# Kernel tuning notes

Measured on AMD Instinct MI355X. Metric: run time of the kernel, lower is better.

The kernel has to match this reference:

```python
import jax, jax.numpy as jnp
import numpy as np

R, TOTAL, N_NODE, B = 4, 32768, 1024, 32
D_IN, D_HID, C, H, NCLS = 256, 256, 8, 8, 10
E = 262144


def setup_inputs() -> dict:
    key = jax.random.key(0)
    ks = jax.random.split(key, 20)
    s = 0.05  # weight scale for numerical stability
    return {
        "h": jax.random.normal(ks[0], (TOTAL, D_IN), jnp.float32),
        "src": jax.random.randint(ks[1], (R, E), 0, TOTAL),
        "dst": jax.random.randint(ks[2], (R, E), 0, TOTAL),
        "node_label": jax.random.randint(ks[3], (TOTAL,), 0, C),
        "feat_label": jax.random.randint(ks[4], (D_HID,), 0, C),
        "W1": jax.random.normal(ks[5], (R, D_IN, D_HID), jnp.float32) * s,
        "b1": jnp.zeros((R, D_HID), jnp.float32),
        "W2": jax.random.normal(ks[6], (R, D_HID, D_HID), jnp.float32) * s,
        "b2": jnp.zeros((R, D_HID), jnp.float32),
        "Wr": jax.random.normal(ks[7], (C, D_HID, D_HID), jnp.float32) * s,
        "br": jnp.zeros((C, D_HID), jnp.float32),
        "Wq": jax.random.normal(ks[8], (D_HID, D_HID), jnp.float32) * s,
        "Wk": jax.random.normal(ks[9], (D_HID, D_HID), jnp.float32) * s,
        "Wv": jax.random.normal(ks[10], (D_HID, D_HID), jnp.float32) * s,
        "lin_w": jax.random.normal(ks[11], (D_HID, D_HID), jnp.float32) * s,
        "lin_b": jnp.zeros((D_HID,), jnp.float32),
        "bn_gamma": jnp.ones((D_HID,), jnp.float32),
        "bn_beta": jnp.zeros((D_HID,), jnp.float32),
        "cls_w": jax.random.normal(ks[12], (NCLS, D_HID), jnp.float32) * s,
        "cls_b": jnp.zeros((NCLS,), jnp.float32),
    }


def _gconv(x, src, dst, W, b, n):
    # DGL GraphConv norm='both' with self-loops added (dgl.add_self_loop)
    loop = jnp.arange(n)
    s = jnp.concatenate([src, loop])
    d = jnp.concatenate([dst, loop])
    ones = jnp.ones(s.shape, jnp.float32)
    deg_out = jnp.maximum(jax.ops.segment_sum(ones, s, num_segments=n), 1.0)
    deg_in = jnp.maximum(jax.ops.segment_sum(ones, d, num_segments=n), 1.0)
    msg = x[s] * jax.lax.rsqrt(deg_out)[s][:, None]          # [E+n, D]
    agg = jax.ops.segment_sum(msg, d, num_segments=n)        # [n, D]
    agg = agg * jax.lax.rsqrt(deg_in)[:, None]
    return agg @ W + b


def _hetero_layer(x, src, dst, W, b, n):
    # HeteroGraphConv: per-relation GraphConv, 'sum' cross-relation aggregation
    out = 0.0
    for r in range(R):
        out = out + _gconv(x, src[r], dst[r], W[r], b[r], n)
    return out


def _attention(x, Wq, Wk, Wv, lin_w, lin_b):
    # FeatureAttentionLayer (eval mode: no attn dropout)
    b, c, d = x.shape
    dh = d // H
    q = (x @ Wq).reshape(b, c, H, dh).transpose(2, 0, 1, 3)   # [H,B,C,dh]
    k = (x @ Wk).reshape(b, c, H, dh).transpose(2, 0, 1, 3)
    v = (x @ Wv).reshape(b, c, H, dh).transpose(2, 0, 1, 3)
    scores = jnp.einsum('hbqd,hbkd->hbqk', q, k) / jnp.sqrt(jnp.float32(c))
    attn = jax.nn.softmax(scores, axis=-1)
    o = jnp.einsum('hbqk,hbkd->hbqd', attn, v)
    o = o.transpose(1, 2, 0, 3).reshape(b, c, d)              # [B,C,D]
    ff = jax.nn.relu(o @ lin_w.T + lin_b) + o                 # feedforward + inner residual
    out = ff + x                                              # outer residual
    return jnp.mean(out, axis=1)                              # [B,D]


def reference(h, src, dst, node_label, feat_label, W1, b1, W2, b2, Wr, br,
              Wq, Wk, Wv, lin_w, lin_b, bn_gamma, bn_beta, cls_w, cls_b):
    n = h.shape[0]
    # RGCN: conv1 -> relu -> conv2
    h1 = jax.nn.relu(_hetero_layer(h, src, dst, W1, b1, n))
    h2 = _hetero_layer(h1, src, dst, W2, b2, n)               # [TOTAL, D_HID]

    node_emb = h2.reshape(B, N_NODE, D_HID)
    node_mask0 = node_label.reshape(B, N_NODE)[0]             # first graph's node types

    # cluster-wise masked pooling + per-cluster linear resize
    pooled = []
    for key in range(C):
        fmask = (feat_label == key).astype(h2.dtype)          # [D]
        nmask = (node_mask0 == key).astype(h2.dtype)          # [N]
        cnt = jnp.maximum(nmask.sum(), 1.0)
        v = jnp.einsum('bnd,n->bd', node_emb, nmask) / cnt    # mean over cluster's nodes
        v = v * fmask[None, :]                                # keep only cluster's features
        pooled.append(v @ Wr[key].T + br[key])
    emb_in = jnp.stack(pooled, axis=1)                        # [B, C, D]

    graph_emb = _attention(emb_in, Wq, Wk, Wv, lin_w, lin_b)  # [B, D]

    hg_raw = jnp.mean(node_emb, axis=1)                       # dgl.mean_nodes per graph
    diff = graph_emb.reshape(-1) - hg_raw.reshape(-1)
    recon = jnp.sqrt(jnp.sum(jnp.square(diff + 1e-6)))        # pairwise_distance p=2

    # BatchNorm1d with batch statistics, dropout identity (eval)
    mu = jnp.mean(graph_emb, axis=0)
    var = jnp.var(graph_emb, axis=0)
    hg = (graph_emb - mu) * jax.lax.rsqrt(var + 1e-5) * bn_gamma + bn_beta
    logits = hg @ cls_w.T + cls_b                             # [B, NCLS]
    return logits, recon
```

## Files before the change

kernel.cpp:

```cpp
#include <hip/hip_runtime.h>
#include <math.h>

#define R_ 4
#define TOTAL_ 32768
#define NNODE_ 1024
#define B_ 32
#define DH_ 256
#define C_ 8
#define H_ 8
#define NCLS_ 10
#define E_ 262144
#define S_ 32
#define CHUNK_ (E_ / S_)

typedef __attribute__((ext_vector_type(8))) short short8v;
typedef __attribute__((ext_vector_type(8))) unsigned short u16x8;
typedef __attribute__((ext_vector_type(4))) float f32x4;
typedef __attribute__((ext_vector_type(2))) float f32x2;
typedef __attribute__((ext_vector_type(2))) unsigned int uint2v;

__device__ inline unsigned short f2bf(float f) {
  unsigned int u = __builtin_bit_cast(unsigned int, f);
  u += 0x7FFF + ((u >> 16) & 1);
  return (unsigned short)(u >> 16);
}
__device__ inline float bf2f(unsigned short s) {
  return __builtin_bit_cast(float, (unsigned int)s << 16);
}


__global__ __launch_bounds__(1024) void hist_part(const int* __restrict__ src,
                                                  const int* __restrict__ dst,
                                                  unsigned int* __restrict__ parts) {
  int r = blockIdx.y, s = blockIdx.x, t = threadIdx.x;
  __shared__ unsigned int hs[16384], hd[16384];
  for (int i = t; i < 16384; i += 1024) { hs[i] = 0; hd[i] = 0; }
  __syncthreads();
  const int* sp = src + (size_t)r * E_ + s * CHUNK_;
  const int* dp = dst + (size_t)r * E_ + s * CHUNK_;
  for (int i = t; i < CHUNK_; i += 1024) {
    int a = sp[i], b = dp[i];
    atomicAdd(&hs[a >> 1], 1u << ((a & 1) * 16));
    atomicAdd(&hd[b >> 1], 1u << ((b & 1) * 16));
  }
  __syncthreads();
  unsigned int* po = parts + ((size_t)(r * S_ + s) * 2) * 16384;
  for (int i = t; i < 16384; i += 1024) { po[i] = hs[i]; po[16384 + i] = hd[i]; }
}

__global__ void reduce_deg(const unsigned int* __restrict__ parts,
                           float* __restrict__ rs_out, float* __restrict__ rs_in,
                           int* __restrict__ cnt_in) {
  int gid = blockIdx.x * 256 + threadIdx.x;
  int r = gid >> 14, w = gid & 16383;
  unsigned int s0 = 0, s1 = 0, d0 = 0, d1 = 0;
  for (int s = 0; s < S_; s++) {
    unsigned int ws_ = parts[((size_t)(r * S_ + s) * 2) * 16384 + w];
    unsigned int wd  = parts[((size_t)(r * S_ + s) * 2 + 1) * 16384 + w];
    s0 += ws_ & 0xffff; s1 += ws_ >> 16;
    d0 += wd & 0xffff;  d1 += wd >> 16;
  }
  int n0 = w * 2, n1 = n0 + 1;
  rs_out[r * TOTAL_ + n0] = rsqrtf((float)(s0 + 1));
  rs_out[r * TOTAL_ + n1] = rsqrtf((float)(s1 + 1));
  rs_in[r * TOTAL_ + n0]  = rsqrtf((float)(d0 + 1));
  rs_in[r * TOTAL_ + n1]  = rsqrtf((float)(d1 + 1));
  cnt_in[r * TOTAL_ + n0] = (int)d0;
  cnt_in[r * TOTAL_ + n1] = (int)d1;
}

__global__ __launch_bounds__(1024) void scan_counts(const int* __restrict__ cnt_in,
                                                    int* __restrict__ off) {
  int r = blockIdx.x;
  const int* c = cnt_in + r * TOTAL_;
  int* o = off + r * (TOTAL_ + 1);
  __shared__ int part[1024];
  int t = threadIdx.x;
  int base = t * 32;
  int loc[32];
  int s = 0;
#pragma unroll
  for (int j = 0; j < 32; j++) { loc[j] = c[base + j]; s += loc[j]; }
  part[t] = s;
  __syncthreads();
  for (int d = 1; d < 1024; d <<= 1) {
    int v = (t >= d) ? part[t - d] : 0;
    __syncthreads();
    part[t] += v;
    __syncthreads();
  }
  int run = (t == 0) ? 0 : part[t - 1];
#pragma unroll
  for (int j = 0; j < 32; j++) {
    o[base + j] = run;
    run += loc[j];
  }
  if (t == 1023) o[TOTAL_] = run;
}

__global__ void base_gen(const unsigned int* __restrict__ parts,
                         const int* __restrict__ csr_off,
                         unsigned int* __restrict__ sbb) {
  int gid = blockIdx.x * 256 + threadIdx.x;
  int r = gid >> 14, w = gid & 16383;
  int n0 = w * 2, n1 = n0 + 1;
  unsigned int run0 = (unsigned int)csr_off[r * (TOTAL_ + 1) + n0];
  unsigned int run1 = (unsigned int)csr_off[r * (TOTAL_ + 1) + n1];
  for (int s = 0; s < S_; s++) {
    unsigned int wd = parts[((size_t)(r * S_ + s) * 2 + 1) * 16384 + w];
    sbb[(size_t)(r * S_ + s) * TOTAL_ + n0] = run0;
    sbb[(size_t)(r * S_ + s) * TOTAL_ + n1] = run1;
    run0 += wd & 0xffff;
    run1 += wd >> 16;
  }
}

__global__ __launch_bounds__(1024) void scatter_csr(const int* __restrict__ src,
                                                    const int* __restrict__ dst,
                                                    const unsigned int* __restrict__ sbb,
                                                    int* __restrict__ csr_src) {
  int r = blockIdx.y, s = blockIdx.x, t = threadIdx.x;
  __shared__ unsigned int basel[TOTAL_];
  const unsigned int* sb = sbb + (size_t)(r * S_ + s) * TOTAL_;
  for (int i = t; i < TOTAL_; i += 1024) basel[i] = sb[i];
  __syncthreads();
  const int* sp = src + (size_t)r * E_ + s * CHUNK_;
  const int* dp = dst + (size_t)r * E_ + s * CHUNK_;
  int* co = csr_src + (size_t)r * E_;
  for (int i = t; i < CHUNK_; i += 1024) {
    int d = dp[i];
    unsigned int slot = atomicAdd(&basel[d], 1u);
    co[slot] = sp[i];
  }
}


__global__ void hconv8(const float* __restrict__ x, unsigned int* __restrict__ xq) {
  size_t i = (size_t)blockIdx.x * blockDim.x + threadIdx.x;
  float4 a = ((const float4*)x)[2 * i];
  float4 b = ((const float4*)x)[2 * i + 1];
  unsigned int lo = 0, hi = 0;
  lo = __builtin_amdgcn_cvt_pk_fp8_f32(a.x, a.y, lo, false);
  lo = __builtin_amdgcn_cvt_pk_fp8_f32(a.z, a.w, lo, true);
  hi = __builtin_amdgcn_cvt_pk_fp8_f32(b.x, b.y, hi, false);
  hi = __builtin_amdgcn_cvt_pk_fp8_f32(b.z, b.w, hi, true);
  uint2v o; o[0] = lo; o[1] = hi;
  *(uint2v*)&xq[2 * i] = o;
}

__global__ void wconv2(const float* __restrict__ W1, const float* __restrict__ W2,
                       unsigned short* __restrict__ T1, unsigned short* __restrict__ T2) {
  int i = blockIdx.x * blockDim.x + threadIdx.x;
  const float* W = (i < 262144) ? W1 : W2;
  unsigned short* T = (i < 262144) ? T1 : T2;
  int j = i & 262143;
  int k = j >> 8, c = j & 255;
  T[(size_t)c * 1024 + k] = f2bf(W[j]);
}

__global__ void bias_sum2(const float* __restrict__ b1, const float* __restrict__ b2,
                          float* __restrict__ s1, float* __restrict__ s2) {
  const float* b = blockIdx.x ? b2 : b1;
  float* s = blockIdx.x ? s2 : s1;
  int d = threadIdx.x;
  s[d] = b[d] + b[DH_ + d] + b[2 * DH_ + d] + b[3 * DH_ + d];
}

__global__ void transpose_mats(const float* __restrict__ Wr, const float* __restrict__ lw,
                               float* __restrict__ Wrt, float* __restrict__ lwt) {
  int i = blockIdx.x * blockDim.x + threadIdx.x;
  int m = i >> 16, j = i & 65535;
  int row = j >> 8, col = j & 255;
  float v = (m < 8) ? Wr[(size_t)m * 65536 + j] : lw[j];
  float* T = (m < 8) ? (Wrt + (size_t)m * 65536) : lwt;
  T[col * 256 + row] = v;
}

__global__ __launch_bounds__(256) void aggregate_f8(
    const unsigned int* __restrict__ xq, const int* __restrict__ csr_off,
    const int* __restrict__ csr_src, const float* __restrict__ rs_out,
    const float* __restrict__ rs_in, unsigned short* __restrict__ aggB) {
  int r = blockIdx.y;
  int node = blockIdx.x * 8 + (threadIdx.x >> 5);
  int lane5 = threadIdx.x & 31;
  const int* offr = csr_off + r * (TOTAL_ + 1);
  const int* srcs = csr_src + (size_t)r * E_;
  const float* rso = rs_out + r * TOTAL_;
  float acc[8];
  {
    uint2v v = *(const uint2v*)&xq[(size_t)node * 64 + lane5 * 2];
    float w = rso[node];
    f32x2 p;
    p = __builtin_amdgcn_cvt_pk_f32_fp8(v[0], false); acc[0] = p[0] * w; acc[1] = p[1] * w;
    p = __builtin_amdgcn_cvt_pk_f32_fp8(v[0], true);  acc[2] = p[0] * w; acc[3] = p[1] * w;
    p = __builtin_amdgcn_cvt_pk_f32_fp8(v[1], false); acc[4] = p[0] * w; acc[5] = p[1] * w;
    p = __builtin_amdgcn_cvt_pk_f32_fp8(v[1], true);  acc[6] = p[0] * w; acc[7] = p[1] * w;
  }
  int e0 = offr[node], e1 = offr[node + 1];
  int e = e0;
  for (; e + 2 <= e1; e += 2) {
    int s0 = srcs[e], s1 = srcs[e + 1];
    uint2v v0 = *(const uint2v*)&xq[(size_t)s0 * 64 + lane5 * 2];
    uint2v v1 = *(const uint2v*)&xq[(size_t)s1 * 64 + lane5 * 2];
    float w0 = rso[s0], w1 = rso[s1];
    f32x2 p;
    p = __builtin_amdgcn_cvt_pk_f32_fp8(v0[0], false); acc[0] += p[0] * w0; acc[1] += p[1] * w0;
    p = __builtin_amdgcn_cvt_pk_f32_fp8(v0[0], true);  acc[2] += p[0] * w0; acc[3] += p[1] * w0;
    p = __builtin_amdgcn_cvt_pk_f32_fp8(v0[1], false); acc[4] += p[0] * w0; acc[5] += p[1] * w0;
    p = __builtin_amdgcn_cvt_pk_f32_fp8(v0[1], true);  acc[6] += p[0] * w0; acc[7] += p[1] * w0;
    p = __builtin_amdgcn_cvt_pk_f32_fp8(v1[0], false); acc[0] += p[0] * w1; acc[1] += p[1] * w1;
    p = __builtin_amdgcn_cvt_pk_f32_fp8(v1[0], true);  acc[2] += p[0] * w1; acc[3] += p[1] * w1;
    p = __builtin_amdgcn_cvt_pk_f32_fp8(v1[1], false); acc[4] += p[0] * w1; acc[5] += p[1] * w1;
    p = __builtin_amdgcn_cvt_pk_f32_fp8(v1[1], true);  acc[6] += p[0] * w1; acc[7] += p[1] * w1;
  }
  if (e < e1) {
    int s0 = srcs[e];
    uint2v v0 = *(const uint2v*)&xq[(size_t)s0 * 64 + lane5 * 2];
    float w0 = rso[s0];
    f32x2 p;
    p = __builtin_amdgcn_cvt_pk_f32_fp8(v0[0], false); acc[0] += p[0] * w0; acc[1] += p[1] * w0;
    p = __builtin_amdgcn_cvt_pk_f32_fp8(v0[0], true);  acc[2] += p[0] * w0; acc[3] += p[1] * w0;
    p = __builtin_amdgcn_cvt_pk_f32_fp8(v0[1], false); acc[4] += p[0] * w0; acc[5] += p[1] * w0;
    p = __builtin_amdgcn_cvt_pk_f32_fp8(v0[1], true);  acc[6] += p[0] * w0; acc[7] += p[1] * w0;
  }
  float wi = rs_in[r * TOTAL_ + node];
  u16x8 o;
#pragma unroll
  for (int j = 0; j < 8; j++) o[j] = f2bf(acc[j] * wi);
  *(u16x8*)&aggB[(size_t)node * 1024 + r * DH_ + lane5 * 8] = o;
}

template <int MODE>
__global__ __launch_bounds__(256) void gemm_mfma(
    const unsigned short* __restrict__ A, const unsigned short* __restrict__ Bt,
    const float* __restrict__ bias, unsigned char* __restrict__ out8,
    unsigned short* __restrict__ out16) {
  __shared__ unsigned short As[128][40];
  __shared__ unsigned short Bs[128][40];
  int t = threadIdx.x;
  int row0 = blockIdx.x * 128, col0 = blockIdx.y * 128;
  int wid = t >> 6, lane = t & 63;
  int wm = wid >> 1, wn = wid & 1;
  int lr = lane & 15, lk = (lane >> 4) * 8;
  f32x4 acc[4][4] = {};
  for (int k0 = 0; k0 < 1024; k0 += 32) {
#pragma unroll
    for (int i = 0; i < 2; i++) {
      int chunk = t + 256 * i;
      int rr = chunk >> 2, kc = (chunk & 3) * 8;
      short8v av = *(const short8v*)&A[(size_t)(row0 + rr) * 1024 + k0 + kc];
      *(short8v*)&As[rr][kc] = av;
      short8v bv = *(const short8v*)&Bt[(size_t)(col0 + rr) * 1024 + k0 + kc];
      *(short8v*)&Bs[rr][kc] = bv;
    }
    __syncthreads();
    short8v afr[4], bfr[4];
#pragma unroll
    for (int m = 0; m < 4; m++) afr[m] = *(const short8v*)&As[wm * 64 + m * 16 + lr][lk];
#pragma unroll
    for (int n = 0; n < 4; n++) bfr[n] = *(const short8v*)&Bs[wn * 64 + n * 16 + lr][lk];
#pragma unroll
    for (int m = 0; m < 4; m++)
#pragma unroll
      for (int n = 0; n < 4; n++)
        acc[m][n] = __builtin_amdgcn_mfma_f32_16x16x32_bf16(afr[m], bfr[n], acc[m][n], 0, 0, 0);
    __syncthreads();
  }
  int lq = lane >> 4;
#pragma unroll
  for (int m = 0; m < 4; m++) {
    int row = row0 + wm * 64 + m * 16 + lq * 4;
#pragma unroll
    for (int n = 0; n < 4; n++) {
      int col = col0 + wn * 64 + n * 16 + lr;
      float bv = bias[col];
#pragma unroll
      for (int q = 0; q < 4; q++) {
        float v = acc[m][n][q] + bv;
        if (MODE == 0) {
          v = fmaxf(v, 0.f);
          int b8 = __builtin_amdgcn_cvt_pk_fp8_f32(v, 0.f, 0, false);
          out8[(size_t)(row + q) * DH_ + col] = (unsigned char)b8;
        } else {
          out16[(size_t)(row + q) * DH_ + col] = f2bf(v);
        }
      }
    }
  }
}


__global__ __launch_bounds__(256) void pool_part(const unsigned short* __restrict__ h2b,
                                                 const int* __restrict__ node_label,
                                                 float* __restrict__ part) {
  int b = blockIdx.x, ch = blockIdx.y, d = threadIdx.x;
  __shared__ int slab[128];
  if (d < 128) slab[d] = node_label[ch * 128 + d];
  __syncthreads();
  float a[C_] = {0.f};
  float at = 0.f;
  const unsigned short* base = h2b + ((size_t)b * NNODE_ + ch * 128) * DH_ + d;
  for (int n = 0; n < 128; n++) {
    float x = bf2f(base[(size_t)n * DH_]);
    int lab = slab[n];
    at += x;
#pragma unroll
    for (int k = 0; k < C_; k++) a[k] += (lab == k) ? x : 0.f;
  }
  float* pb = part + ((size_t)(ch * B_ + b) * 9) * DH_ + d;
#pragma unroll
  for (int k = 0; k < C_; k++) pb[(size_t)k * DH_] = a[k];
  pb[(size_t)8 * DH_] = at;
}

__global__ __launch_bounds__(256) void pool_fin(const float* __restrict__ part,
                                                const int* __restrict__ node_label,
                                                const int* __restrict__ feat_label,
                                                float* __restrict__ poolv,
                                                float* __restrict__ hg_raw) {
  int b = blockIdx.x, d = threadIdx.x;
  __shared__ int cnt[C_];
  if (d < C_) cnt[d] = 0;
  __syncthreads();
  for (int n = d; n < NNODE_; n += 256) atomicAdd(&cnt[node_label[n]], 1);
  __syncthreads();
  float s[9];
#pragma unroll
  for (int k = 0; k < 9; k++) s[k] = 0.f;
  for (int ch = 0; ch < 8; ch++) {
    const float* pb = part + ((size_t)(ch * B_ + b) * 9) * DH_ + d;
#pragma unroll
    for (int k = 0; k < 9; k++) s[k] += pb[(size_t)k * DH_];
  }
  int fl = feat_label[d];
#pragma unroll
  for (int k = 0; k < C_; k++) {
    float cntf = fmaxf((float)cnt[k], 1.f);
    float v = (fl == k) ? (s[k] / cntf) : 0.f;
    poolv[((size_t)k * B_ + b) * DH_ + d] = v;
  }
  hg_raw[(size_t)b * DH_ + d] = s[8] * (1.f / NNODE_);
}


__global__ __launch_bounds__(256) void resize_t(const float* __restrict__ poolv,
                                                const float* __restrict__ Wrt,
                                                const float* __restrict__ br,
                                                float* __restrict__ emb) {
  int key = blockIdx.x & 7, b = blockIdx.x >> 3, t = threadIdx.x;
  __shared__ float pl[DH_];
  pl[t] = poolv[((size_t)key * B_ + b) * DH_ + t];
  __syncthreads();
  const float* W = Wrt + (size_t)key * DH_ * DH_;
  float s = 0.f;
  for (int d = 0; d < DH_; d++) s += pl[d] * W[d * DH_ + t];
  emb[((size_t)b * C_ + key) * DH_ + t] = s + br[key * DH_ + t];
}

__global__ __launch_bounds__(256) void qkv_t(const float* __restrict__ emb,
                                             const float* __restrict__ Wq,
                                             const float* __restrict__ Wk,
                                             const float* __restrict__ Wv,
                                             float* __restrict__ q, float* __restrict__ k,
                                             float* __restrict__ v) {
  int idx = blockIdx.x, t = threadIdx.x;
  __shared__ float x[DH_];
  x[t] = emb[(size_t)idx * DH_ + t];
  __syncthreads();
  float sq = 0.f, sk = 0.f, sv = 0.f;
  for (int kk = 0; kk < DH_; kk++) {
    float xv = x[kk];
    sq += xv * Wq[kk * DH_ + t];
    sk += xv * Wk[kk * DH_ + t];
    sv += xv * Wv[kk * DH_ + t];
  }
  q[(size_t)idx * DH_ + t] = sq;
  k[(size_t)idx * DH_ + t] = sk;
  v[(size_t)idx * DH_ + t] = sv;
}

__global__ __launch_bounds__(256) void attn_core(const float* __restrict__ q,
                                                 const float* __restrict__ k,
                                                 const float* __restrict__ v,
                                                 float* __restrict__ osb) {
  int b = blockIdx.x, t = threadIdx.x;
  __shared__ float qs[C_][DH_], ks[C_][DH_], vs[C_][DH_];
  __shared__ float sc[H_][C_][C_];
  for (int c = 0; c < C_; c++) {
    qs[c][t] = q[((size_t)b * C_ + c) * DH_ + t];
    ks[c][t] = k[((size_t)b * C_ + c) * DH_ + t];
    vs[c][t] = v[((size_t)b * C_ + c) * DH_ + t];
  }
  __syncthreads();
  for (int idx = t; idx < H_ * C_ * C_; idx += 256) {
    int hh = idx / (C_ * C_);
    int qc = (idx / C_) % C_;
    int kc = idx % C_;
    float s = 0.f;
    for (int dd = 0; dd < 32; dd++) s += qs[qc][hh * 32 + dd] * ks[kc][hh * 32 + dd];
    sc[hh][qc][kc] = s * 0.35355339059327373f;
  }
  __syncthreads();
  if (t < H_ * C_) {
    int hh = t / C_, qc = t % C_;
    float m = -1e30f;
    for (int kc = 0; kc < C_; kc++) m = fmaxf(m, sc[hh][qc][kc]);
    float sum = 0.f;
    for (int kc = 0; kc < C_; kc++) { float e = expf(sc[hh][qc][kc] - m); sc[hh][qc][kc] = e; sum += e; }
    float inv = 1.f / sum;
    for (int kc = 0; kc < C_; kc++) sc[hh][qc][kc] *= inv;
  }
  __syncthreads();
  int hh = t >> 5;
  for (int c = 0; c < C_; c++) {
    float s = 0.f;
#pragma unroll
    for (int kc = 0; kc < C_; kc++) s += sc[hh][c][kc] * vs[kc][t];
    osb[((size_t)b * C_ + c) * DH_ + t] = s;
  }
}

__global__ __launch_bounds__(256) void ff_res(const float* __restrict__ osb,
                                              const float* __restrict__ emb,
                                              const float* __restrict__ lwt,
                                              const float* __restrict__ lb,
                                              float* __restrict__ ffb) {
  int idx = blockIdx.x, t = threadIdx.x;
  __shared__ float ox[DH_];
  ox[t] = osb[(size_t)idx * DH_ + t];
  __syncthreads();
  float s = 0.f;
  for (int d = 0; d < DH_; d++) s += ox[d] * lwt[d * DH_ + t];
  ffb[(size_t)idx * DH_ + t] =
      fmaxf(s + lb[t], 0.f) + ox[t] + emb[(size_t)idx * DH_ + t];
}

__global__ __launch_bounds__(256) void tail_final(
    const float* __restrict__ ffb, const float* __restrict__ hg_raw,
    const float* __restrict__ g, const float* __restrict__ be,
    const float* __restrict__ cw, const float* __restrict__ cb,
    float* __restrict__ out) {
  int t = threadIdx.x;
  __shared__ float hgn[B_][DH_];
  __shared__ float red[256];
  float gcol[B_];
  float mu = 0.f;
#pragma unroll
  for (int b = 0; b < B_; b++) {
    float s = 0.f;
    for (int c = 0; c < C_; c++) s += ffb[((size_t)b * C_ + c) * DH_ + t];
    gcol[b] = s * (1.f / C_);
    mu += gcol[b];
  }
  mu *= (1.f / B_);
  float var = 0.f;
#pragma unroll
  for (int b = 0; b < B_; b++) { float x = gcol[b] - mu; var += x * x; }
  var *= (1.f / B_);
  float is = rsqrtf(var + 1e-5f);
  float gm = g[t], bt = be[t];
  float s = 0.f;
#pragma unroll
  for (int b = 0; b < B_; b++) {
    hgn[b][t] = (gcol[b] - mu) * is * gm + bt;
    float d = gcol[b] - hg_raw[b * DH_ + t] + 1e-6f;
    s += d * d;
  }
  red[t] = s;
  __syncthreads();
  for (int w = 128; w > 0; w >>= 1) {
    if (t < w) red[t] += red[t + w];
    __syncthreads();
  }
  if (t == 0) out[B_ * NCLS_] = sqrtf(red[0]);
  for (int o = t; o < B_ * NCLS_; o += 256) {
    int b = o / NCLS_, j = o % NCLS_;
    float sl = cb[j];
    for (int d = 0; d < DH_; d++) sl += hgn[b][d] * cw[j * DH_ + d];
    out[o] = sl;
  }
}


extern "C" void kernel_launch(void* const* d_in, const int* in_sizes, int n_in,
                              void* d_out, int out_size, void* d_ws, size_t ws_size,
                              hipStream_t stream) {
  const float* h   = (const float*)d_in[0];
  const int* src   = (const int*)d_in[1];
  const int* dst   = (const int*)d_in[2];
  const int* nlab  = (const int*)d_in[3];
  const int* flab  = (const int*)d_in[4];
  const float* W1  = (const float*)d_in[5];
  const float* b1  = (const float*)d_in[6];
  const float* W2  = (const float*)d_in[7];
  const float* b2  = (const float*)d_in[8];
  const float* Wr  = (const float*)d_in[9];
  const float* br  = (const float*)d_in[10];
  const float* Wq  = (const float*)d_in[11];
  const float* Wk  = (const float*)d_in[12];
  const float* Wv  = (const float*)d_in[13];
  const float* lw  = (const float*)d_in[14];
  const float* lb  = (const float*)d_in[15];
  const float* bng = (const float*)d_in[16];
  const float* bnb = (const float*)d_in[17];
  const float* cw  = (const float*)d_in[18];
  const float* cb  = (const float*)d_in[19];
  float* out = (float*)d_out;

  char* p = (char*)d_ws;
  auto alloc = [&](size_t bytes) -> void* {
    void* q = (void*)p;
    p += (bytes + 255) & ~(size_t)255;
    return q;
  };
  unsigned int* xq    = (unsigned int*)alloc((size_t)TOTAL_ * DH_);
  unsigned char* h1q  = (unsigned char*)alloc((size_t)TOTAL_ * DH_);
  unsigned short* h2b = (unsigned short*)alloc((size_t)TOTAL_ * DH_ * 2);
  unsigned short* aggB = (unsigned short*)alloc((size_t)TOTAL_ * 1024 * 2);
  unsigned short* Wt1  = (unsigned short*)alloc((size_t)1024 * DH_ * 2);
  unsigned short* Wt2  = (unsigned short*)alloc((size_t)1024 * DH_ * 2);
  float* Wrt   = (float*)alloc((size_t)C_ * DH_ * DH_ * 4);
  float* lwt   = (float*)alloc((size_t)DH_ * DH_ * 4);
  float* bsum1 = (float*)alloc(DH_ * 4);
  float* bsum2 = (float*)alloc(DH_ * 4);
  int* cnt_in   = (int*)alloc((size_t)R_ * TOTAL_ * 4);
  float* rs_out = (float*)alloc((size_t)R_ * TOTAL_ * 4);
  float* rs_in  = (float*)alloc((size_t)R_ * TOTAL_ * 4);
  int* csr_off  = (int*)alloc((size_t)R_ * (TOTAL_ + 1) * 4);
  int* csr_src  = (int*)alloc((size_t)R_ * E_ * 4);
  float* part   = (float*)alloc((size_t)8 * B_ * 9 * DH_ * 4);
  float* poolv  = (float*)alloc((size_t)C_ * B_ * DH_ * 4);
  float* hg_raw = (float*)alloc((size_t)B_ * DH_ * 4);
  float* emb    = (float*)alloc((size_t)B_ * C_ * DH_ * 4);
  float* qb     = (float*)alloc((size_t)B_ * C_ * DH_ * 4);
  float* kb     = (float*)alloc((size_t)B_ * C_ * DH_ * 4);
  float* vb     = (float*)alloc((size_t)B_ * C_ * DH_ * 4);
  float* osb    = (float*)alloc((size_t)B_ * C_ * DH_ * 4);
  float* ffb    = (float*)alloc((size_t)B_ * C_ * DH_ * 4);

  unsigned int* parts = (unsigned int*)aggB;
  unsigned int* sbb   = (unsigned int*)((char*)aggB + (size_t)16 * 1024 * 1024);

  hist_part<<<dim3(S_, R_), 1024, 0, stream>>>(src, dst, parts);
  reduce_deg<<<R_ * TOTAL_ / 512, 256, 0, stream>>>(parts, rs_out, rs_in, cnt_in);
  scan_counts<<<R_, 1024, 0, stream>>>(cnt_in, csr_off);
  base_gen<<<R_ * TOTAL_ / 512, 256, 0, stream>>>(parts, csr_off, sbb);
  scatter_csr<<<dim3(S_, R_), 1024, 0, stream>>>(src, dst, sbb, csr_src);

  wconv2<<<2048, 256, 0, stream>>>(W1, W2, Wt1, Wt2);
  bias_sum2<<<2, 256, 0, stream>>>(b1, b2, bsum1, bsum2);
  transpose_mats<<<9 * 256, 256, 0, stream>>>(Wr, lw, Wrt, lwt);
  hconv8<<<TOTAL_ * DH_ / 8 / 256, 256, 0, stream>>>(h, xq);

  aggregate_f8<<<dim3(TOTAL_ / 8, R_), 256, 0, stream>>>(xq, csr_off, csr_src, rs_out, rs_in, aggB);
  gemm_mfma<0><<<dim3(TOTAL_ / 128, 2), 256, 0, stream>>>(aggB, Wt1, bsum1, h1q, nullptr);

  aggregate_f8<<<dim3(TOTAL_ / 8, R_), 256, 0, stream>>>((const unsigned int*)h1q, csr_off, csr_src, rs_out, rs_in, aggB);
  gemm_mfma<1><<<dim3(TOTAL_ / 128, 2), 256, 0, stream>>>(aggB, Wt2, bsum2, nullptr, h2b);

  pool_part<<<dim3(B_, 8), 256, 0, stream>>>(h2b, nlab, part);
  pool_fin<<<B_, 256, 0, stream>>>(part, nlab, flab, poolv, hg_raw);
  resize_t<<<B_ * C_, 256, 0, stream>>>(poolv, Wrt, br, emb);
  qkv_t<<<B_ * C_, 256, 0, stream>>>(emb, Wq, Wk, Wv, qb, kb, vb);
  attn_core<<<B_, 256, 0, stream>>>(qb, kb, vb, osb);
  ff_res<<<B_ * C_, 256, 0, stream>>>(osb, emb, lwt, lb, ffb);
  tail_final<<<1, 256, 0, stream>>>(ffb, hg_raw, bng, bnb, cw, cb, out);
}
```

Measured before the change: 320.7 us.

## Switch aggregation output and layer GEMMs from bf16 to fp8 MFMA

The aggregation kernel now writes its normalized sums as fp8 instead of bf16, using one 64-lane wave per node. Both layer GEMMs consume these fp8 inputs with fp8-quantized weights through the fp8 MFMA instruction, processing 64-wide K steps. This halves the aggregation write traffic and the GEMM read traffic and uses the higher-throughput fp8 matrix path, at the cost of extra quantization error on aggregated features and weights. The resize and QKV projection kernels are also fused into one launch, which removes an emb round trip.

Measured after the change: 330.1 us. 1.03x slower.

```diff
diff --git a/kernel.cpp b/kernel.cpp
--- a/kernel.cpp
+++ b/kernel.cpp
@@ -13,11 +13,11 @@
 #define S_ 32
 #define CHUNK_ (E_ / S_)
 
-typedef __attribute__((ext_vector_type(8))) short short8v;
-typedef __attribute__((ext_vector_type(8))) unsigned short u16x8;
 typedef __attribute__((ext_vector_type(4))) float f32x4;
 typedef __attribute__((ext_vector_type(2))) float f32x2;
 typedef __attribute__((ext_vector_type(2))) unsigned int uint2v;
+typedef __attribute__((ext_vector_type(4))) unsigned int uint4v;
+typedef long long i64;
 
 __device__ inline unsigned short f2bf(float f) {
   unsigned int u = __builtin_bit_cast(unsigned int, f);
@@ -148,14 +148,22 @@
   *(uint2v*)&xq[2 * i] = o;
 }
 
-__global__ void wconv2(const float* __restrict__ W1, const float* __restrict__ W2,
-                       unsigned short* __restrict__ T1, unsigned short* __restrict__ T2) {
-  int i = blockIdx.x * blockDim.x + threadIdx.x;
-  const float* W = (i < 262144) ? W1 : W2;
-  unsigned short* T = (i < 262144) ? T1 : T2;
-  int j = i & 262143;
-  int k = j >> 8, c = j & 255;
-  T[(size_t)c * 1024 + k] = f2bf(W[j]);
+__global__ void wconv_f8(const float* __restrict__ W1, const float* __restrict__ W2,
+                         unsigned int* __restrict__ T1, unsigned int* __restrict__ T2) {
+  int id = blockIdx.x * blockDim.x + threadIdx.x;
+  const float* W = (id < 65536) ? W1 : W2;
+  unsigned int* T = (id < 65536) ? T1 : T2;
+  int j = id & 65535;
+  int c = j >> 8, kq = j & 255;
+  int k0 = kq * 4;
+  float w0 = W[(size_t)(k0 + 0) * 256 + c];
+  float w1 = W[(size_t)(k0 + 1) * 256 + c];
+  float w2 = W[(size_t)(k0 + 2) * 256 + c];
+  float w3 = W[(size_t)(k0 + 3) * 256 + c];
+  unsigned int o = 0;
+  o = __builtin_amdgcn_cvt_pk_fp8_f32(w0, w1, o, false);
+  o = __builtin_amdgcn_cvt_pk_fp8_f32(w2, w3, o, true);
+  T[(size_t)c * 256 + kq] = o;
 }
 
 __global__ void bias_sum2(const float* __restrict__ b1, const float* __restrict__ b2,
@@ -179,91 +187,90 @@
 __global__ __launch_bounds__(256) void aggregate_f8(
     const unsigned int* __restrict__ xq, const int* __restrict__ csr_off,
     const int* __restrict__ csr_src, const float* __restrict__ rs_out,
-    const float* __restrict__ rs_in, unsigned short* __restrict__ aggB) {
+    const float* __restrict__ rs_in, unsigned int* __restrict__ aggQ) {
   int r = blockIdx.y;
-  int node = blockIdx.x * 8 + (threadIdx.x >> 5);
-  int lane5 = threadIdx.x & 31;
+  int node = blockIdx.x * 4 + (threadIdx.x >> 6);
+  int lane = threadIdx.x & 63;
   const int* offr = csr_off + r * (TOTAL_ + 1);
   const int* srcs = csr_src + (size_t)r * E_;
   const float* rso = rs_out + r * TOTAL_;
-  float acc[8];
+  float a0, a1, a2, a3;
   {
-    uint2v v = *(const uint2v*)&xq[(size_t)node * 64 + lane5 * 2];
+    unsigned int v = xq[(size_t)node * 64 + lane];
     float w = rso[node];
-    f32x2 p;
-    p = __builtin_amdgcn_cvt_pk_f32_fp8(v[0], false); acc[0] = p[0] * w; acc[1] = p[1] * w;
-    p = __builtin_amdgcn_cvt_pk_f32_fp8(v[0], true);  acc[2] = p[0] * w; acc[3] = p[1] * w;
-    p = __builtin_amdgcn_cvt_pk_f32_fp8(v[1], false); acc[4] = p[0] * w; acc[5] = p[1] * w;
-    p = __builtin_amdgcn_cvt_pk_f32_fp8(v[1], true);  acc[6] = p[0] * w; acc[7] = p[1] * w;
+    f32x2 p0 = __builtin_amdgcn_cvt_pk_f32_fp8(v, false);
+    f32x2 p1 = __builtin_amdgcn_cvt_pk_f32_fp8(v, true);
+    a0 = p0[0] * w; a1 = p0[1] * w; a2 = p1[0] * w; a3 = p1[1] * w;
   }
   int e0 = offr[node], e1 = offr[node + 1];
   int e = e0;
-  for (; e + 2 <= e1; e += 2) {
-    int s0 = srcs[e], s1 = srcs[e + 1];
-    uint2v v0 = *(const uint2v*)&xq[(size_t)s0 * 64 + lane5 * 2];
-    uint2v v1 = *(const uint2v*)&xq[(size_t)s1 * 64 + lane5 * 2];
-    float w0 = rso[s0], w1 = rso[s1];
+  for (; e + 4 <= e1; e += 4) {
+    int s0 = srcs[e], s1 = srcs[e + 1], s2 = srcs[e + 2], s3 = srcs[e + 3];
+    unsigned int v0 = xq[(size_t)s0 * 64 + lane];
+    unsigned int v1 = xq[(size_t)s1 * 64 + lane];
+    unsigned int v2 = xq[(size_t)s2 * 64 + lane];
+    unsigned int v3 = xq[(size_t)s3 * 64 + lane];
+    float w0 = rso[s0], w1 = rso[s1], w2 = rso[s2], w3 = rso[s3];
     f32x2 p;
-    p = __builtin_amdgcn_cvt_pk_f32_fp8(v0[0], false); acc[0] += p[0] * w0; acc[1] += p[1] * w0;
-    p = __builtin_amdgcn_cvt_pk_f32_fp8(v0[0], true);  acc[2] += p[0] * w0; acc[3] += p[1] * w0;
-    p = __builtin_amdgcn_cvt_pk_f32_fp8(v0[1], false); acc[4] += p[0] * w0; acc[5] += p[1] * w0;
-    p = __builtin_amdgcn_cvt_pk_f32_fp8(v0[1], true);  acc[6] += p[0] * w0; acc[7] += p[1] * w0;
-    p = __builtin_amdgcn_cvt_pk_f32_fp8(v1[0], false); acc[0] += p[0] * w1; acc[1] += p[1] * w1;
-    p = __builtin_amdgcn_cvt_pk_f32_fp8(v1[0], true);  acc[2] += p[0] * w1; acc[3] += p[1] * w1;
-    p = __builtin_amdgcn_cvt_pk_f32_fp8(v1[1], false); acc[4] += p[0] * w1; acc[5] += p[1] * w1;
-    p = __builtin_amdgcn_cvt_pk_f32_fp8(v1[1], true);  acc[6] += p[0] * w1; acc[7] += p[1] * w1;
-  }
-  if (e < e1) {
+    p = __builtin_amdgcn_cvt_pk_f32_fp8(v0, false); a0 += p[0] * w0; a1 += p[1] * w0;
+    p = __builtin_amdgcn_cvt_pk_f32_fp8(v0, true);  a2 += p[0] * w0; a3 += p[1] * w0;
+    p = __builtin_amdgcn_cvt_pk_f32_fp8(v1, false); a0 += p[0] * w1; a1 += p[1] * w1;
+    p = __builtin_amdgcn_cvt_pk_f32_fp8(v1, true);  a2 += p[0] * w1; a3 += p[1] * w1;
+    p = __builtin_amdgcn_cvt_pk_f32_fp8(v2, false); a0 += p[0] * w2; a1 += p[1] * w2;
+    p = __builtin_amdgcn_cvt_pk_f32_fp8(v2, true);  a2 += p[0] * w2; a3 += p[1] * w2;
+    p = __builtin_amdgcn_cvt_pk_f32_fp8(v3, false); a0 += p[0] * w3; a1 += p[1] * w3;
+    p = __builtin_amdgcn_cvt_pk_f32_fp8(v3, true);  a2 += p[0] * w3; a3 += p[1] * w3;
+  }
+  for (; e < e1; e++) {
     int s0 = srcs[e];
-    uint2v v0 = *(const uint2v*)&xq[(size_t)s0 * 64 + lane5 * 2];
+    unsigned int v0 = xq[(size_t)s0 * 64 + lane];
     float w0 = rso[s0];
     f32x2 p;
-    p = __builtin_amdgcn_cvt_pk_f32_fp8(v0[0], false); acc[0] += p[0] * w0; acc[1] += p[1] * w0;
-    p = __builtin_amdgcn_cvt_pk_f32_fp8(v0[0], true);  acc[2] += p[0] * w0; acc[3] += p[1] * w0;
-    p = __builtin_amdgcn_cvt_pk_f32_fp8(v0[1], false); acc[4] += p[0] * w0; acc[5] += p[1] * w0;
-    p = __builtin_amdgcn_cvt_pk_f32_fp8(v0[1], true);  acc[6] += p[0] * w0; acc[7] += p[1] * w0;
+    p = __builtin_amdgcn_cvt_pk_f32_fp8(v0, false); a0 += p[0] * w0; a1 += p[1] * w0;
+    p = __builtin_amdgcn_cvt_pk_f32_fp8(v0, true);  a2 += p[0] * w0; a3 += p[1] * w0;
   }
   float wi = rs_in[r * TOTAL_ + node];
-  u16x8 o;
-#pragma unroll
-  for (int j = 0; j < 8; j++) o[j] = f2bf(acc[j] * wi);
-  *(u16x8*)&aggB[(size_t)node * 1024 + r * DH_ + lane5 * 8] = o;
+  unsigned int o = 0;
+  o = __builtin_amdgcn_cvt_pk_fp8_f32(a0 * wi, a1 * wi, o, false);
+  o = __builtin_amdgcn_cvt_pk_fp8_f32(a2 * wi, a3 * wi, o, true);
+  aggQ[(size_t)node * 256 + r * 64 + lane] = o;
 }
 
 template <int MODE>
-__global__ __launch_bounds__(256) void gemm_mfma(
-    const unsigned short* __restrict__ A, const unsigned short* __restrict__ Bt,
+__global__ __launch_bounds__(256) void gemm_f8(
+    const unsigned char* __restrict__ A, const unsigned char* __restrict__ Bt,
     const float* __restrict__ bias, unsigned char* __restrict__ out8,
     unsigned short* __restrict__ out16) {
-  __shared__ unsigned short As[128][40];
-  __shared__ unsigned short Bs[128][40];
+  __shared__ unsigned char As[128][80];
+  __shared__ unsigned char Bs[128][80];
   int t = threadIdx.x;
   int row0 = blockIdx.x * 128, col0 = blockIdx.y * 128;
   int wid = t >> 6, lane = t & 63;
   int wm = wid >> 1, wn = wid & 1;
-  int lr = lane & 15, lk = (lane >> 4) * 8;
+  int lr = lane & 15, lk = lane >> 4;
   f32x4 acc[4][4] = {};
-  for (int k0 = 0; k0 < 1024; k0 += 32) {
+  for (int k0 = 0; k0 < 1024; k0 += 64) {
 #pragma unroll
     for (int i = 0; i < 2; i++) {
-      int chunk = t + 256 * i;
-      int rr = chunk >> 2, kc = (chunk & 3) * 8;
-      short8v av = *(const short8v*)&A[(size_t)(row0 + rr) * 1024 + k0 + kc];
-      *(short8v*)&As[rr][kc] = av;
-      short8v bv = *(const short8v*)&Bt[(size_t)(col0 + rr) * 1024 + k0 + kc];
-      *(short8v*)&Bs[rr][kc] = bv;
+      int c = t + 256 * i;
+      int rr = c >> 2, cc = (c & 3) * 16;
+      *(uint4v*)&As[rr][cc] = *(const uint4v*)&A[(size_t)(row0 + rr) * 1024 + k0 + cc];
+      *(uint4v*)&Bs[rr][cc] = *(const uint4v*)&Bt[(size_t)(col0 + rr) * 1024 + k0 + cc];
     }
     __syncthreads();
-    short8v afr[4], bfr[4];
-#pragma unroll
-    for (int m = 0; m < 4; m++) afr[m] = *(const short8v*)&As[wm * 64 + m * 16 + lr][lk];
-#pragma unroll
-    for (int n = 0; n < 4; n++) bfr[n] = *(const short8v*)&Bs[wn * 64 + n * 16 + lr][lk];
-#pragma unroll
-    for (int m = 0; m < 4; m++)
-#pragma unroll
-      for (int n = 0; n < 4; n++)
-        acc[m][n] = __builtin_amdgcn_mfma_f32_16x16x32_bf16(afr[m], bfr[n], acc[m][n], 0, 0, 0);
+#pragma unroll
+    for (int kk = 0; kk < 2; kk++) {
+      i64 afr[4], bfr[4];
+#pragma unroll
+      for (int m = 0; m < 4; m++) afr[m] = *(const i64*)&As[wm * 64 + m * 16 + lr][kk * 32 + lk * 8];
+#pragma unroll
+      for (int n = 0; n < 4; n++) bfr[n] = *(const i64*)&Bs[wn * 64 + n * 16 + lr][kk * 32 + lk * 8];
+#pragma unroll
+      for (int m = 0; m < 4; m++)
+#pragma unroll
+        for (int n = 0; n < 4; n++)
+          acc[m][n] = __builtin_amdgcn_mfma_f32_16x16x32_fp8_fp8(afr[m], bfr[n], acc[m][n], 0, 0, 0);
+    }
     __syncthreads();
   }
   int lq = lane >> 4;
@@ -343,40 +350,37 @@
 }
 
 
-__global__ __launch_bounds__(256) void resize_t(const float* __restrict__ poolv,
-                                                const float* __restrict__ Wrt,
-                                                const float* __restrict__ br,
-                                                float* __restrict__ emb) {
+__global__ __launch_bounds__(256) void rq_t(const float* __restrict__ poolv,
+                                            const float* __restrict__ Wrt,
+                                            const float* __restrict__ br,
+                                            const float* __restrict__ Wq,
+                                            const float* __restrict__ Wk,
+                                            const float* __restrict__ Wv,
+                                            float* __restrict__ emb,
+                                            float* __restrict__ q, float* __restrict__ k,
+                                            float* __restrict__ v) {
   int key = blockIdx.x & 7, b = blockIdx.x >> 3, t = threadIdx.x;
-  __shared__ float pl[DH_];
+  __shared__ float pl[DH_], es[DH_];
   pl[t] = poolv[((size_t)key * B_ + b) * DH_ + t];
   __syncthreads();
   const float* W = Wrt + (size_t)key * DH_ * DH_;
   float s = 0.f;
   for (int d = 0; d < DH_; d++) s += pl[d] * W[d * DH_ + t];
-  emb[((size_t)b * C_ + key) * DH_ + t] = s + br[key * DH_ + t];
-}
-
-__global__ __launch_bounds__(256) void qkv_t(const float* __restrict__ emb,
-                                             const float* __restrict__ Wq,
-                                             const float* __restrict__ Wk,
-                                             const float* __restrict__ Wv,
-                                             float* __restrict__ q, float* __restrict__ k,
-                                             float* __restrict__ v) {
-  int idx = blockIdx.x, t = threadIdx.x;
-  __shared__ float x[DH_];
-  x[t] = emb[(size_t)idx * DH_ + t];
+  s += br[key * DH_ + t];
+  es[t] = s;
+  size_t idx = (size_t)b * C_ + key;
+  emb[idx * DH_ + t] = s;
   __syncthreads();
   float sq = 0.f, sk = 0.f, sv = 0.f;
   for (int kk = 0; kk < DH_; kk++) {
-    float xv = x[kk];
+    float xv = es[kk];
     sq += xv * Wq[kk * DH_ + t];
     sk += xv * Wk[kk * DH_ + t];
     sv += xv * Wv[kk * DH_ + t];
   }
-  q[(size_t)idx * DH_ + t] = sq;
-  k[(size_t)idx * DH_ + t] = sk;
-  v[(size_t)idx * DH_ + t] = sv;
+  q[idx * DH_ + t] = sq;
+  k[idx * DH_ + t] = sk;
+  v[idx * DH_ + t] = sv;
 }
 
 __global__ __launch_bounds__(256) void attn_core(const float* __restrict__ q,
@@ -514,11 +518,11 @@
     return q;
   };
   unsigned int* xq    = (unsigned int*)alloc((size_t)TOTAL_ * DH_);
-  unsigned char* h1q  = (unsigned char*)alloc((size_t)TOTAL_ * DH_);
+  unsigned int* h1q   = (unsigned int*)alloc((size_t)TOTAL_ * DH_);
   unsigned short* h2b = (unsigned short*)alloc((size_t)TOTAL_ * DH_ * 2);
-  unsigned short* aggB = (unsigned short*)alloc((size_t)TOTAL_ * 1024 * 2);
-  unsigned short* Wt1  = (unsigned short*)alloc((size_t)1024 * DH_ * 2);
-  unsigned short* Wt2  = (unsigned short*)alloc((size_t)1024 * DH_ * 2);
+  unsigned int* aggQ  = (unsigned int*)alloc((size_t)TOTAL_ * 1024);
+  unsigned int* Wq1   = (unsigned int*)alloc((size_t)256 * 256 * 4);
+  unsigned int* Wq2   = (unsigned int*)alloc((size_t)256 * 256 * 4);
   float* Wrt   = (float*)alloc((size_t)C_ * DH_ * DH_ * 4);
   float* lwt   = (float*)alloc((size_t)DH_ * DH_ * 4);
   float* bsum1 = (float*)alloc(DH_ * 4);
@@ -538,8 +542,8 @@
   float* osb    = (float*)alloc((size_t)B_ * C_ * DH_ * 4);
   float* ffb    = (float*)alloc((size_t)B_ * C_ * DH_ * 4);
 
-  unsigned int* parts = (unsigned int*)aggB;
-  unsigned int* sbb   = (unsigned int*)((char*)aggB + (size_t)16 * 1024 * 1024);
+  unsigned int* parts = aggQ;
+  unsigned int* sbb   = (unsigned int*)((char*)aggQ + (size_t)16 * 1024 * 1024);
 
   hist_part<<<dim3(S_, R_), 1024, 0, stream>>>(src, dst, parts);
   reduce_deg<<<R_ * TOTAL_ / 512, 256, 0, stream>>>(parts, rs_out, rs_in, cnt_in);
@@ -547,21 +551,24 @@
   base_gen<<<R_ * TOTAL_ / 512, 256, 0, stream>>>(parts, csr_off, sbb);
   scatter_csr<<<dim3(S_, R_), 1024, 0, stream>>>(src, dst, sbb, csr_src);
 
-  wconv2<<<2048, 256, 0, stream>>>(W1, W2, Wt1, Wt2);
+  wconv_f8<<<512, 256, 0, stream>>>(W1, W2, Wq1, Wq2);
   bias_sum2<<<2, 256, 0, stream>>>(b1, b2, bsum1, bsum2);
   transpose_mats<<<9 * 256, 256, 0, stream>>>(Wr, lw, Wrt, lwt);
   hconv8<<<TOTAL_ * DH_ / 8 / 256, 256, 0, stream>>>(h, xq);
 
-  aggregate_f8<<<dim3(TOTAL_ / 8, R_), 256, 0, stream>>>(xq, csr_off, csr_src, rs_out, rs_in, aggB);
-  gemm_mfma<0><<<dim3(TOTAL_ / 128, 2), 256, 0, stream>>>(aggB, Wt1, bsum1, h1q, nullptr);
-
-  aggregate_f8<<<dim3(TOTAL_ / 8, R_), 256, 0, stream>>>((const unsigned int*)h1q, csr_off, csr_src, rs_out, rs_in, aggB);
-  gemm_mfma<1><<<dim3(TOTAL_ / 128, 2), 256, 0, stream>>>(aggB, Wt2, bsum2, nullptr, h2b);
+  aggregate_f8<<<dim3(TOTAL_ / 4, R_), 256, 0, stream>>>(xq, csr_off, csr_src, rs_out, rs_in, aggQ);
+  gemm_f8<0><<<dim3(TOTAL_ / 128, 2), 256, 0, stream>>>(
+      (const unsigned char*)aggQ, (const unsigned char*)Wq1, bsum1,
+      (unsigned char*)h1q, nullptr);
+
+  aggregate_f8<<<dim3(TOTAL_ / 4, R_), 256, 0, stream>>>(h1q, csr_off, csr_src, rs_out, rs_in, aggQ);
+  gemm_f8<1><<<dim3(TOTAL_ / 128, 2), 256, 0, stream>>>(
+      (const unsigned char*)aggQ, (const unsigned char*)Wq2, bsum2,
+      nullptr, h2b);
 
   pool_part<<<dim3(B_, 8), 256, 0, stream>>>(h2b, nlab, part);
   pool_fin<<<B_, 256, 0, stream>>>(part, nlab, flab, poolv, hg_raw);
-  resize_t<<<B_ * C_, 256, 0, stream>>>(poolv, Wrt, br, emb);
-  qkv_t<<<B_ * C_, 256, 0, stream>>>(emb, Wq, Wk, Wv, qb, kb, vb);
+  rq_t<<<B_ * C_, 256, 0, stream>>>(poolv, Wrt, br, Wq, Wk, Wv, emb, qb, kb, vb);
   attn_core<<<B_, 256, 0, stream>>>(qb, kb, vb, osb);
   ff_res<<<B_ * C_, 256, 0, stream>>>(osb, emb, lwt, lb, ffb);
   tail_final<<<1, 256, 0, stream>>>(ffb, hg_raw, bng, bnb, cw, cb, out);
```
